# Optimization experiments

Measured on AMD Instinct MI355X. Metric: run time of the kernel, lower is better.

The kernel has to match this reference:

```python
import jax, jax.numpy as jnp
import numpy as np

T = 16000        # signal length
N1 = 120         # first-order filters (J=12, Q=10)
NPSI2 = 14       # second-order filterbank size (Q2=1)
NPAIR = 553      # second-order coefficients -> 120 + 553 = 673 channels
SUB1 = 8         # subsample U1 before order 2
T2 = T // SUB1   # 2000
STR1 = 1000      # lowpass stride at length T  -> 16 output samples
STR2 = T2 // (T // STR1)  # 125 -> 16 output samples
LOG_EPS = 1e-6
BN_EPS = 1e-5


def _gauss_hat(N, xi, sigma):
    om = np.arange(N) / N
    return np.exp(-((om - xi) ** 2) / (2.0 * sigma ** 2)).astype(np.float32)


def _filterbank():
    Q = 10.0
    xi1 = 0.45 * 2.0 ** (-np.arange(N1) / Q)
    sig1 = np.maximum(xi1 * 0.1, 2.0 / T)
    psi1 = np.stack([_gauss_hat(T, x, s) for x, s in zip(xi1, sig1)])
    phi1 = _gauss_hat(T, 0.0, 0.4 / STR1)
    xi2 = 0.45 * 2.0 ** (-np.arange(NPSI2, dtype=np.float64))
    sig2 = np.maximum(xi2 * 0.2, 2.0 / T2)
    psi2 = np.stack([_gauss_hat(T2, x, s) for x, s in zip(xi2, sig2)])
    phi2 = _gauss_hat(T2, 0.0, 0.4 / STR2)
    pairs = [(i, j) for i in range(N1) for j in range(NPSI2) if xi2[j] < xi1[i] / 2.0]
    pairs = pairs[:NPAIR]
    assert len(pairs) == NPAIR
    pi1 = np.array([p[0] for p in pairs], np.int32)
    pi2 = np.array([p[1] for p in pairs], np.int32)
    return psi1, phi1, psi2, phi2, pi1, pi2


def setup_inputs():
    key = jax.random.key(0)
    ks = jax.random.split(key, 8)
    psi1, phi1, psi2, phi2, pi1, pi2 = _filterbank()
    B = 32
    inp = {
        "x": jax.random.normal(ks[0], (B, 1, T), jnp.float32),
        "psi1_hat": jnp.asarray(psi1),
        "phi1_hat": jnp.asarray(phi1),
        "psi2_hat": jnp.asarray(psi2),
        "phi2_hat": jnp.asarray(phi2),
        "gamma": jnp.ones((673,), jnp.float32),
        "beta": jnp.zeros((673,), jnp.float32),
        "W1": jax.random.normal(ks[1], (300, 673), jnp.float32) * 0.04,
        "b1": jnp.zeros((300,), jnp.float32),
        "W2": jax.random.normal(ks[2], (90, 300), jnp.float32) * 0.06,
        "b2": jnp.zeros((90,), jnp.float32),
        "W3": jax.random.normal(ks[3], (35, 90), jnp.float32) * 0.1,
        "b3": jnp.zeros((35,), jnp.float32),
        "pair_i1": jnp.asarray(pi1),
        "pair_i2": jnp.asarray(pi2),
    }
    return inp


def reference(x, psi1_hat, phi1_hat, psi2_hat, phi2_hat, gamma, beta,
              W1, b1, W2, b2, W3, b3, pair_i1, pair_i2):
    xs = x.squeeze(1)                                       # [B, T]
    Xf = jnp.fft.fft(xs)                                    # [B, T] c64
    # --- order 1: wavelet conv (freq-domain), modulus ---
    U1 = jnp.abs(jnp.fft.ifft(Xf[:, None, :] * psi1_hat[None]))        # [B, N1, T]
    # S1 = lowpass(U1) subsampled to 16 samples
    S1 = jnp.real(jnp.fft.ifft(jnp.fft.fft(U1) * phi1_hat))[..., ::STR1]  # [B, N1, 16]
    # --- order 2 on subsampled U1 ---
    U1sf = jnp.fft.fft(U1[..., ::SUB1])                     # [B, N1, T2]
    U2 = jnp.abs(jnp.fft.ifft(U1sf[:, pair_i1, :] * psi2_hat[pair_i2]))  # [B, NPAIR, T2]
    S2 = jnp.real(jnp.fft.ifft(jnp.fft.fft(U2) * phi2_hat))[..., ::STR2]  # [B, NPAIR, 16]
    S = jnp.concatenate([S1, S2], axis=1)                   # [B, 673, 16]
    # log-abs + temporal mean pooling
    f = jnp.mean(jnp.log(jnp.abs(S) + LOG_EPS), axis=-1)    # [B, 673]
    # BatchNorm1d (training mode: batch statistics)
    mu = jnp.mean(f, axis=0)
    var = jnp.var(f, axis=0)
    f = (f - mu) / jnp.sqrt(var + BN_EPS) * gamma + beta
    # MLP head
    h = jax.nn.relu(f @ W1.T + b1)
    h = jax.nn.relu(h @ W2.T + b2)
    return jax.nn.log_softmax(h @ W3.T + b3, axis=-1)
```

## Files before the change

### kernel.cpp

```cpp
#include <hip/hip_runtime.h>
#include <math.h>

typedef float2 cf;

__device__ __forceinline__ cf cadd(cf a, cf b){ return make_float2(a.x+b.x, a.y+b.y); }
__device__ __forceinline__ cf csub(cf a, cf b){ return make_float2(a.x-b.x, a.y-b.y); }
__device__ __forceinline__ cf cmul(cf a, cf b){ return make_float2(a.x*b.x - a.y*b.y, a.x*b.y + a.y*b.x); }

__device__ __forceinline__ int SW(int i){ return i ^ ((i>>4)&15); }
#define AT(x) s[SW(x)]
#define WFENCE asm volatile("" ::: "memory")

template<bool WAVE> __device__ __forceinline__ void SYf(){
  if constexpr (WAVE) { WFENCE; } else __syncthreads();
}

__device__ __forceinline__ int devB(int i){
  int jm = i/10 + 2;
  double kc = 900.0*exp2((double)(-jm));
  double sg = fmax(180.0*exp2((double)(-jm)), 2.0);
  return min(2000, (int)ceil(kc + 6.5*sg) + 1);
}

template<int N, int L, bool INV>
__device__ __forceinline__ void stage_r2(cf* __restrict__ s, const cf* __restrict__ tw, int tid, int nt){
  constexpr int Ls = L/2, nbf = N/2, tws = 16000/L;
  for (int q = tid; q < nbf; q += nt){
    int blk = q / Ls, j = q - blk*Ls;
    int base = blk*L + j;
    cf w1 = tw[tws*j]; if (INV) w1.y = -w1.y;
    if (!INV){
      cf a = AT(base), b = AT(base+Ls);
      AT(base) = cadd(a,b);
      AT(base+Ls) = cmul(csub(a,b), w1);
    } else {
      cf a = AT(base), b = cmul(AT(base+Ls), w1);
      AT(base) = cadd(a,b);
      AT(base+Ls) = csub(a,b);
    }
  }
}

template<int N, int L, bool INV>
__device__ __forceinline__ void stage_r4(cf* __restrict__ s, const cf* __restrict__ tw, int tid, int nt){
  constexpr int Ls = L/4, nbf = N/4, tws = 16000/L;
  for (int q = tid; q < nbf; q += nt){
    int blk = q / Ls, j = q - blk*Ls;
    int base = blk*L + j;
    cf w1 = tw[tws*j]; if (INV) w1.y = -w1.y;
    cf w2 = cmul(w1,w1), w3 = cmul(w2,w1);
    if (!INV){
      cf y0=AT(base), y1=AT(base+Ls), y2=AT(base+2*Ls), y3=AT(base+3*Ls);
      cf t0=cadd(y0,y2), t1=csub(y0,y2), t2=cadd(y1,y3), t3=csub(y1,y3);
      AT(base)      = cadd(t0,t2);
      AT(base+Ls)   = cmul(make_float2(t1.x + t3.y, t1.y - t3.x), w1);
      AT(base+2*Ls) = cmul(csub(t0,t2), w2);
      AT(base+3*Ls) = cmul(make_float2(t1.x - t3.y, t1.y + t3.x), w3);
    } else {
      cf z0=AT(base);
      cf z1=cmul(AT(base+Ls),   w1);
      cf z2=cmul(AT(base+2*Ls), w2);
      cf z3=cmul(AT(base+3*Ls), w3);
      cf t0=cadd(z0,z2), t1=csub(z0,z2), t2=cadd(z1,z3), t3=csub(z1,z3);
      AT(base)      = cadd(t0,t2);
      AT(base+Ls)   = make_float2(t1.x - t3.y, t1.y + t3.x);
      AT(base+2*Ls) = csub(t0,t2);
      AT(base+3*Ls) = make_float2(t1.x + t3.y, t1.y - t3.x);
    }
  }
}

template<int N, int L, bool INV>
__device__ __forceinline__ void stage_r5(cf* __restrict__ s, const cf* __restrict__ tw, int tid, int nt){
  constexpr int Ls = L/5, nbf = N/5, tws = 16000/L;
  const float C1 = 0.30901699437494742f, S1c = 0.95105651629515357f;
  const float C2 = -0.80901699437494745f, S2c = 0.58778525229247314f;
  for (int q = tid; q < nbf; q += nt){
    int blk = q / Ls, j = q - blk*Ls;
    int base = blk*L + j;
    cf w1 = tw[tws*j]; if (INV) w1.y = -w1.y;
    cf w2 = cmul(w1,w1), w3 = cmul(w2,w1), w4 = cmul(w2,w2);
    if (!INV){
      cf y0=AT(base), y1=AT(base+Ls), y2=AT(base+2*Ls), y3=AT(base+3*Ls), y4=AT(base+4*Ls);
      cf t1=cadd(y1,y4), t2=csub(y1,y4), t3=cadd(y2,y3), t4=csub(y2,y3);
      cf z0 = cadd(y0, cadd(t1,t3));
      cf m1 = make_float2(y0.x + C1*t1.x + C2*t3.x, y0.y + C1*t1.y + C2*t3.y);
      cf m2 = make_float2(y0.x + C2*t1.x + C1*t3.x, y0.y + C2*t1.y + C1*t3.y);
      cf wa = make_float2(S1c*t2.x + S2c*t4.x, S1c*t2.y + S2c*t4.y);
      cf wb = make_float2(S2c*t2.x - S1c*t4.x, S2c*t2.y - S1c*t4.y);
      cf o1 = make_float2(m1.x + wa.y, m1.y - wa.x);
      cf o4 = make_float2(m1.x - wa.y, m1.y + wa.x);
      cf o2 = make_float2(m2.x + wb.y, m2.y - wb.x);
      cf o3 = make_float2(m2.x - wb.y, m2.y + wb.x);
      AT(base) = z0;
      AT(base+Ls)   = cmul(o1,w1);
      AT(base+2*Ls) = cmul(o2,w2);
      AT(base+3*Ls) = cmul(o3,w3);
      AT(base+4*Ls) = cmul(o4,w4);
    } else {
      cf z0=AT(base);
      cf z1=cmul(AT(base+Ls),   w1);
      cf z2=cmul(AT(base+2*Ls), w2);
      cf z3=cmul(AT(base+3*Ls), w3);
      cf z4=cmul(AT(base+4*Ls), w4);
      cf t1=cadd(z1,z4), t2=csub(z1,z4), t3=cadd(z2,z3), t4=csub(z2,z3);
      cf y0 = cadd(z0, cadd(t1,t3));
      cf m1 = make_float2(z0.x + C1*t1.x + C2*t3.x, z0.y + C1*t1.y + C2*t3.y);
      cf m2 = make_float2(z0.x + C2*t1.x + C1*t3.x, z0.y + C2*t1.y + C1*t3.y);
      cf wa = make_float2(S1c*t2.x + S2c*t4.x, S1c*t2.y + S2c*t4.y);
      cf wb = make_float2(S2c*t2.x - S1c*t4.x, S2c*t2.y - S1c*t4.y);
      AT(base)      = y0;
      AT(base+Ls)   = make_float2(m1.x - wa.y, m1.y + wa.x);
      AT(base+2*Ls) = make_float2(m2.x - wb.y, m2.y + wb.x);
      AT(base+3*Ls) = make_float2(m2.x + wb.y, m2.y - wb.x);
      AT(base+4*Ls) = make_float2(m1.x + wa.y, m1.y - wa.x);
    }
  }
}

template<int N, int L, bool INV>
__device__ __forceinline__ void stage_r8(cf* __restrict__ s, const cf* __restrict__ tw, int tid, int nt){
  constexpr int Ls = L/8, nbf = N/8, tws = 16000/L;
  const float RC = 0.70710678118654752f;
  for (int q = tid; q < nbf; q += nt){
    int blk = q / Ls, j = q - blk*Ls;
    int base = blk*L + j;
    cf w1 = tw[tws*j]; if (INV) w1.y = -w1.y;
    cf w2 = cmul(w1,w1), w3 = cmul(w2,w1), w4 = cmul(w2,w2);
    cf w5 = cmul(w4,w1), w6 = cmul(w3,w3), w7 = cmul(w4,w3);
    if (!INV){
      cf y0=AT(base), y1=AT(base+Ls), y2=AT(base+2*Ls), y3=AT(base+3*Ls);
      cf y4=AT(base+4*Ls), y5=AT(base+5*Ls), y6=AT(base+6*Ls), y7=AT(base+7*Ls);
      cf b0=cadd(y0,y4), b1=csub(y0,y4);
      cf b2=cadd(y2,y6), b3=csub(y2,y6);
      cf b4=cadd(y1,y5), b5=csub(y1,y5);
      cf b6=cadd(y3,y7), b7=csub(y3,y7);
      cf r3 = make_float2(b3.y, -b3.x);
      cf r7 = make_float2(b7.y, -b7.x);
      cf c0=cadd(b0,b2), c1=csub(b0,b2);
      cf c2=cadd(b1,r3), c3=csub(b1,r3);
      cf c4=cadd(b4,b6), c5=csub(b4,b6);
      cf c6=cadd(b5,r7), c7=csub(b5,r7);
      cf r5 = make_float2(c5.y, -c5.x);
      cf wc6 = make_float2(RC*(c6.x + c6.y), RC*(c6.y - c6.x));
      cf wc7 = make_float2(RC*(c7.y - c7.x), RC*(-c7.y - c7.x));
      AT(base)      = cadd(c0,c4);
      AT(base+Ls)   = cmul(cadd(c2,wc6), w1);
      AT(base+2*Ls) = cmul(cadd(c1,r5),  w2);
      AT(base+3*Ls) = cmul(cadd(c3,wc7), w3);
      AT(base+4*Ls) = cmul(csub(c0,c4),  w4);
      AT(base+5*Ls) = cmul(csub(c2,wc6), w5);
      AT(base+6*Ls) = cmul(csub(c1,r5),  w6);
      AT(base+7*Ls) = cmul(csub(c3,wc7), w7);
    } else {
      cf z0=AT(base);
      cf z1=cmul(AT(base+Ls),   w1);
      cf z2=cmul(AT(base+2*Ls), w2);
      cf z3=cmul(AT(base+3*Ls), w3);
      cf z4=cmul(AT(base+4*Ls), w4);
      cf z5=cmul(AT(base+5*Ls), w5);
      cf z6=cmul(AT(base+6*Ls), w6);
      cf z7=cmul(AT(base+7*Ls), w7);
      cf b0=cadd(z0,z4), b1=csub(z0,z4);
      cf b2=cadd(z2,z6), b3=csub(z2,z6);
      cf b4=cadd(z1,z5), b5=csub(z1,z5);
      cf b6=cadd(z3,z7), b7=csub(z3,z7);
      cf r3 = make_float2(-b3.y, b3.x);
      cf r7 = make_float2(-b7.y, b7.x);
      cf c0=cadd(b0,b2), c1=csub(b0,b2);
      cf c2=cadd(b1,r3), c3=csub(b1,r3);
      cf c4=cadd(b4,b6), c5=csub(b4,b6);
      cf c6=cadd(b5,r7), c7=csub(b5,r7);
      cf r5 = make_float2(-c5.y, c5.x);
      cf wc6 = make_float2(RC*(c6.x - c6.y), RC*(c6.x + c6.y));
      cf wc7 = make_float2(RC*(-c7.x - c7.y), RC*(c7.x - c7.y));
      AT(base)      = cadd(c0,c4);
      AT(base+Ls)   = cadd(c2,wc6);
      AT(base+2*Ls) = cadd(c1,r5);
      AT(base+3*Ls) = cadd(c3,wc7);
      AT(base+4*Ls) = csub(c0,c4);
      AT(base+5*Ls) = csub(c2,wc6);
      AT(base+6*Ls) = csub(c1,r5);
      AT(base+7*Ls) = csub(c3,wc7);
    }
  }
}

template<bool INV>
__device__ void fft16000(cf* s, const cf* tw, int tid, int nt){
  if (!INV){
    stage_r5<16000,16000,false>(s,tw,tid,nt); __syncthreads();
    stage_r5<16000, 3200,false>(s,tw,tid,nt); __syncthreads();
    stage_r5<16000,  640,false>(s,tw,tid,nt); __syncthreads();
    stage_r8<16000,  128,false>(s,tw,tid,nt); __syncthreads();
    stage_r4<16000,   16,false>(s,tw,tid,nt); __syncthreads();
    stage_r4<16000,    4,false>(s,tw,tid,nt); __syncthreads();
  } else {
    stage_r4<16000,    4,true >(s,tw,tid,nt); __syncthreads();
    stage_r4<16000,   16,true >(s,tw,tid,nt); __syncthreads();
    stage_r8<16000,  128,true >(s,tw,tid,nt); __syncthreads();
    stage_r5<16000,  640,true >(s,tw,tid,nt); __syncthreads();
    stage_r5<16000, 3200,true >(s,tw,tid,nt); __syncthreads();
    stage_r5<16000,16000,true >(s,tw,tid,nt); __syncthreads();
  }
}

template<bool INV>
__device__ void fft2000(cf* s, const cf* tw, int tid, int nt){
  if (!INV){
    stage_r5<2000,2000,false>(s,tw,tid,nt); __syncthreads();
    stage_r5<2000, 400,false>(s,tw,tid,nt); __syncthreads();
    stage_r5<2000,  80,false>(s,tw,tid,nt); __syncthreads();
    stage_r4<2000,  16,false>(s,tw,tid,nt); __syncthreads();
    stage_r4<2000,   4,false>(s,tw,tid,nt); __syncthreads();
  } else {
    stage_r4<2000,   4,true >(s,tw,tid,nt); __syncthreads();
    stage_r4<2000,  16,true >(s,tw,tid,nt); __syncthreads();
    stage_r5<2000,  80,true >(s,tw,tid,nt); __syncthreads();
    stage_r5<2000, 400,true >(s,tw,tid,nt); __syncthreads();
    stage_r5<2000,2000,true >(s,tw,tid,nt); __syncthreads();
  }
}

__device__ void fft8000i(cf* s, const cf* tw, int tid, int nt){
  stage_r8<8000,   8,true>(s,tw,tid,nt); __syncthreads();
  stage_r8<8000,  64,true>(s,tw,tid,nt); __syncthreads();
  stage_r5<8000, 320,true>(s,tw,tid,nt); __syncthreads();
  stage_r5<8000,1600,true>(s,tw,tid,nt); __syncthreads();
  stage_r5<8000,8000,true>(s,tw,tid,nt); __syncthreads();
}
__device__ void fft4000i(cf* s, const cf* tw, int tid, int nt){
  stage_r4<4000,   4,true>(s,tw,tid,nt); __syncthreads();
  stage_r8<4000,  32,true>(s,tw,tid,nt); __syncthreads();
  stage_r5<4000, 160,true>(s,tw,tid,nt); __syncthreads();
  stage_r5<4000, 800,true>(s,tw,tid,nt); __syncthreads();
  stage_r5<4000,4000,true>(s,tw,tid,nt); __syncthreads();
}
__device__ void fft500i(cf* s, const cf* tw, int tid, int nt){
  stage_r4<500,  4,true>(s,tw,tid,nt); __syncthreads();
  stage_r5<500, 20,true>(s,tw,tid,nt); __syncthreads();
  stage_r5<500,100,true>(s,tw,tid,nt); __syncthreads();
  stage_r5<500,500,true>(s,tw,tid,nt); __syncthreads();
}
__device__ void fft1000i(cf* s, const cf* tw, int tid, int nt){
  stage_r8<1000,   8,true>(s,tw,tid,nt); __syncthreads();
  stage_r5<1000,  40,true>(s,tw,tid,nt); __syncthreads();
  stage_r5<1000, 200,true>(s,tw,tid,nt); __syncthreads();
  stage_r5<1000,1000,true>(s,tw,tid,nt); __syncthreads();
}
__device__ __forceinline__ void fft250w(cf* s, const cf* tw, int lane){
  stage_r2<250,  2,true>(s,tw,lane,64); WFENCE;
  stage_r5<250, 10,true>(s,tw,lane,64); WFENCE;
  stage_r5<250, 50,true>(s,tw,lane,64); WFENCE;
  stage_r5<250,250,true>(s,tw,lane,64); WFENCE;
}
__device__ __forceinline__ void fft125w(cf* s, const cf* tw, int lane){
  stage_r5<125,  5,true>(s,tw,lane,64); WFENCE;
  stage_r5<125, 25,true>(s,tw,lane,64); WFENCE;
  stage_r5<125,125,true>(s,tw,lane,64); WFENCE;
}

template<int M, bool INV, bool WAVE>
__device__ __forceinline__ void fftg(cf* s, const cf* tw, int tid, int nt){
  if constexpr (M==2000){
    if constexpr (INV){
      stage_r4<2000,4,true>(s,tw,tid,nt); SYf<WAVE>();
      stage_r4<2000,16,true>(s,tw,tid,nt); SYf<WAVE>();
      stage_r5<2000,80,true>(s,tw,tid,nt); SYf<WAVE>();
      stage_r5<2000,400,true>(s,tw,tid,nt); SYf<WAVE>();
      stage_r5<2000,2000,true>(s,tw,tid,nt); SYf<WAVE>();
    } else {
      stage_r5<2000,2000,false>(s,tw,tid,nt); SYf<WAVE>();
      stage_r5<2000,400,false>(s,tw,tid,nt); SYf<WAVE>();
      stage_r5<2000,80,false>(s,tw,tid,nt); SYf<WAVE>();
      stage_r4<2000,16,false>(s,tw,tid,nt); SYf<WAVE>();
      stage_r4<2000,4,false>(s,tw,tid,nt); SYf<WAVE>();
    }
  } else if constexpr (M==1600){
    if constexpr (INV){
      stage_r8<1600,8,true>(s,tw,tid,nt); SYf<WAVE>();
      stage_r8<1600,64,true>(s,tw,tid,nt); SYf<WAVE>();
      stage_r5<1600,320,true>(s,tw,tid,nt); SYf<WAVE>();
      stage_r5<1600,1600,true>(s,tw,tid,nt); SYf<WAVE>();
    } else {
      stage_r5<1600,1600,false>(s,tw,tid,nt); SYf<WAVE>();
      stage_r5<1600,320,false>(s,tw,tid,nt); SYf<WAVE>();
      stage_r8<1600,64,false>(s,tw,tid,nt); SYf<WAVE>();
      stage_r8<1600,8,false>(s,tw,tid,nt); SYf<WAVE>();
    }
  } else if constexpr (M==640){
    if constexpr (INV){
      stage_r4<640,4,true>(s,tw,tid,nt); SYf<WAVE>();
      stage_r4<640,16,true>(s,tw,tid,nt); SYf<WAVE>();
      stage_r8<640,128,true>(s,tw,tid,nt); SYf<WAVE>();
      stage_r5<640,640,true>(s,tw,tid,nt); SYf<WAVE>();
    } else {
      stage_r5<640,640,false>(s,tw,tid,nt); SYf<WAVE>();
      stage_r8<640,128,false>(s,tw,tid,nt); SYf<WAVE>();
      stage_r4<640,16,false>(s,tw,tid,nt); SYf<WAVE>();
      stage_r4<640,4,false>(s,tw,tid,nt); SYf<WAVE>();
    }
  } else if constexpr (M==320){
    if constexpr (INV){
      stage_r8<320,8,true>(s,tw,tid,nt); SYf<WAVE>();
      stage_r8<320,64,true>(s,tw,tid,nt); SYf<WAVE>();
      stage_r5<320,320,true>(s,tw,tid,nt); SYf<WAVE>();
    } else {
      stage_r5<320,320,false>(s,tw,tid,nt); SYf<WAVE>();
      stage_r8<320,64,false>(s,tw,tid,nt); SYf<WAVE>();
      stage_r8<320,8,false>(s,tw,tid,nt); SYf<WAVE>();
    }
  } else if constexpr (M==200){
    if constexpr (INV){
      stage_r8<200,8,true>(s,tw,tid,nt); SYf<WAVE>();
      stage_r5<200,40,true>(s,tw,tid,nt); SYf<WAVE>();
      stage_r5<200,200,true>(s,tw,tid,nt); SYf<WAVE>();
    } else {
      stage_r5<200,200,false>(s,tw,tid,nt); SYf<WAVE>();
      stage_r5<200,40,false>(s,tw,tid,nt); SYf<WAVE>();
      stage_r8<200,8,false>(s,tw,tid,nt); SYf<WAVE>();
    }
  } else {
    if constexpr (INV){
      stage_r4<160,4,true>(s,tw,tid,nt); SYf<WAVE>();
      stage_r8<160,32,true>(s,tw,tid,nt); SYf<WAVE>();
      stage_r5<160,160,true>(s,tw,tid,nt); SYf<WAVE>();
    } else {
      stage_r5<160,160,false>(s,tw,tid,nt); SYf<WAVE>();
      stage_r8<160,32,false>(s,tw,tid,nt); SYf<WAVE>();
      stage_r4<160,4,false>(s,tw,tid,nt); SYf<WAVE>();
    }
  }
}

__device__ __forceinline__ int pos16000(int k){
  int k0=k%5; k/=5; int k1=k%5; k/=5; int k2=k%5; k/=5;
  int k3=k&7; k>>=3; int k4=k&3; k>>=2;
  return k0*3200 + k1*640 + k2*128 + k3*16 + k4*4 + k;
}
__device__ __forceinline__ int pos8000(int k){
  int k0=k%5; k/=5; int k1=k%5; k/=5; int k2=k%5; k/=5;
  int k3=k&7, k4=k>>3;
  return k0*1600 + k1*320 + k2*64 + k3*8 + k4;
}
__device__ __forceinline__ int pos4000(int k){
  int k0=k%5; k/=5; int k1=k%5; k/=5; int k2=k%5; k/=5;
  int k3=k&7, k4=k>>3;
  return k0*800 + k1*160 + k2*32 + k3*4 + k4;
}
__device__ __forceinline__ int pos2000(int k){
  int k0=k%5; k/=5; int k1=k%5; k/=5; int k2=k%5; k/=5;
  int k3=k&3, k4=k>>2;
  return k0*400 + k1*80 + k2*16 + k3*4 + k4;
}
__device__ __forceinline__ int pos1600(int k){
  int k0=k%5; k/=5; int k1=k%5; k/=5;
  int k2=k&7; k>>=3;
  return k0*320 + k1*64 + k2*8 + k;
}
__device__ __forceinline__ int pos1000(int k){
  int k0=k%5; k/=5; int k1=k%5; k/=5; int k2=k%5; k/=5;
  return k0*200 + k1*40 + k2*8 + k;
}
__device__ __forceinline__ int pos640(int k){
  int k0=k%5; k/=5;
  int k1=k&7; k>>=3; int k2=k&3; k>>=2;
  return k0*128 + k1*16 + k2*4 + k;
}
__device__ __forceinline__ int pos500(int k){
  int k0=k%5; k/=5; int k1=k%5; k/=5; int k2=k%5; k/=5;
  return k0*100 + k1*20 + k2*4 + k;
}
__device__ __forceinline__ int pos320(int k){
  int k0=k%5; k/=5;
  int k1=k&7; k>>=3;
  return k0*64 + k1*8 + k;
}
__device__ __forceinline__ int pos250(int k){
  int k0=k%5; k/=5; int k1=k%5; k/=5; int k2=k%5; k/=5;
  return k0*50 + k1*10 + k2*2 + k;
}
__device__ __forceinline__ int pos125(int k){
  int k0=k%5; k/=5; int k1=k%5; k/=5;
  return k0*25 + k1*5 + k;
}
__device__ __forceinline__ int pos200(int k){
  int k0=k%5; k/=5; int k1=k%5; k/=5;
  return k0*40 + k1*8 + k;
}
__device__ __forceinline__ int pos160(int k){
  int k0=k%5; k/=5;
  int k1=k&7; k>>=3;
  return k0*32 + k1*4 + k;
}

template<int M> __device__ __forceinline__ int posM(int k){
  if constexpr (M==16000) return pos16000(k);
  else if constexpr (M==8000) return pos8000(k);
  else if constexpr (M==4000) return pos4000(k);
  else return pos2000(k);
}
template<int M> __device__ __forceinline__ int posN(int k){
  if constexpr (M==2000) return pos2000(k);
  else if constexpr (M==1600) return pos1600(k);
  else if constexpr (M==640) return pos640(k);
  else if constexpr (M==320) return pos320(k);
  else if constexpr (M==200) return pos200(k);
  else return pos160(k);
}
template<int M> __device__ __forceinline__ void fftM_inv(cf* s, const cf* tw, int tid, int nt){
  if constexpr (M==16000) fft16000<true>(s,tw,tid,nt);
  else if constexpr (M==8000) fft8000i(s,tw,tid,nt);
  else if constexpr (M==4000) fft4000i(s,tw,tid,nt);
  else fft2000<true>(s,tw,tid,nt);
}


__global__ void k_tw(cf* __restrict__ tw){
  int j = blockIdx.x*blockDim.x + threadIdx.x;
  if (j < 16000){
    double a = -6.283185307179586476925286766559 * (double)j / 16000.0;
    tw[j] = make_float2((float)cos(a), (float)sin(a));
  }
}

__global__ void k_btab(const float* __restrict__ phi1, const float* __restrict__ phi2,
                       float* __restrict__ h1g, float* __restrict__ h2g){
  int i = blockIdx.x*blockDim.x + threadIdx.x;
  const double TWO_PI = 6.283185307179586476925286766559;
  if (i < 5201){
    int d = i - 2600;
    double a = 0.0;
    for (int k = 0; k < 64; ++k) a += (double)phi1[k]*cos(TWO_PI*(double)(k*d)/16000.0);
    h1g[i] = (float)(a/16000.0 - (double)phi1[0]/32000.0);
  } else if (i == 5201){
    h1g[5201] = phi1[0]*(1.f/32000.f);
  } else if (i < 5202 + 661){
    int j = i - 5202; int d = j - 330;
    double a = 0.0;
    for (int k = 0; k < 64; ++k) a += (double)phi2[k]*cos(TWO_PI*(double)(k*d)/2000.0);
    h2g[j] = (float)(a/2000.0 - (double)phi2[0]/4000.0);
  } else if (i == 5202 + 661){
    h2g[661] = phi2[0]*(1.f/4000.f);
  }
}

__global__ __launch_bounds__(1024) void k_classify(const int* __restrict__ pi2,
                                                   int* __restrict__ list5, int* __restrict__ list4){
  __shared__ int w5[16], w4[16];
  int p = threadIdx.x;
  for (int t = p; t < 493; t += 1024) list5[t] = 0;
  for (int t = p; t < 60;  t += 1024) list4[t] = 0;
  bool valid = p < 553;
  int j2 = valid ? pi2[p] : 99;
  bool f5 = valid && (j2 >= 5);
  bool f4 = valid && (j2 < 5);
  unsigned long long m5 = __ballot(f5);
  unsigned long long m4 = __ballot(f4);
  int lane = p & 63, wid = p >> 6;
  if (lane == 0){ w5[wid] = __popcll(m5); w4[wid] = __popcll(m4); }
  __syncthreads();
  if (valid){
    int b5 = 0, b4 = 0;
    for (int w = 0; w < wid; ++w){ b5 += w5[w]; b4 += w4[w]; }
    unsigned long long lm = (1ull << lane) - 1ull;
    if (f5) list5[b5 + __popcll(m5 & lm)] = p;
    if (f4) list4[b4 + __popcll(m4 & lm)] = p;
  }
}

__global__ __launch_bounds__(1024) void k_fftx(const float* __restrict__ x, cf* __restrict__ Xf,
                                               const cf* __restrict__ tw){
  extern __shared__ cf s[];
  int b = blockIdx.x;
  int tid = threadIdx.x, nt = blockDim.x;
  for (int n = tid; n < 16000; n += nt) AT(n) = make_float2(x[b*16000 + n], 0.f);
  __syncthreads();
  fft16000<false>(s, tw, tid, nt);
  for (int k = tid; k < 16000; k += nt) Xf[b*16000 + k] = AT(pos16000(k));
}

template<int M, int ST, int NF, int I0, int NT>
__global__ __launch_bounds__(NT) void kf(const cf* __restrict__ Xf, const float* __restrict__ psi1,
                                         const float* __restrict__ h1g, const cf* __restrict__ tw,
                                         cf* __restrict__ U1sf, float* __restrict__ S1){
  extern __shared__ cf s[];
  constexpr int NW = NT/64;
  int b = blockIdx.x / NF;
  int i = I0 + (blockIdx.x - b*NF);
  int tid = threadIdx.x, wid = tid>>6, lane = tid&63;
  double x1 = 0.45 * exp2((double)(-i) / 10.0);
  double kc = 16000.0 * x1;
  double sg = fmax(1600.0 * x1, 2.0);
  int k0 = max(0, (int)floor(kc - 6.5*sg));
  int k1 = min(16000, (int)ceil(kc + 6.5*sg) + 1);
  int W = k1 - k0;
  for (int n = tid; n < M; n += NT) s[n] = make_float2(0.f, 0.f);
  __syncthreads();
  const cf* X = Xf + (size_t)b*16000 + k0;
  const float* P = psi1 + (size_t)i*16000 + k0;
  for (int j = tid; j < W; j += NT){
    cf v = X[j]; float pf = P[j];
    int pp = posM<M>(j);
    AT(pp) = make_float2(v.x*pf, v.y*pf);
  }
  __syncthreads();
  fftM_inv<M>(s, tw, tid, NT);
  constexpr int R = (M + NT - 1)/NT;
  float mreg[R]; float tsum = 0.f;
  const float inv = 1.f/16000.f;
  #pragma unroll
  for (int r = 0; r < R; ++r){
    int n = tid + r*NT;
    if (n < M){ cf v = AT(n); mreg[r] = sqrtf(v.x*v.x + v.y*v.y)*inv; tsum += mreg[r]; }
    else mreg[r] = 0.f;
  }
  float* fl = (float*)s;
  float* part = (float*)(s + M);
  __syncthreads();
  #pragma unroll
  for (int r = 0; r < R; ++r){ int n = tid + r*NT; if (n < M) fl[n] = mreg[r]; }
  #pragma unroll
  for (int o = 32; o > 0; o >>= 1) tsum += __shfl_xor(tsum, o);
  if (lane == 0) part[wid] = tsum;
  __syncthreads();
  if (tid == 0){ float tt = 0.f; for (int w = 0; w < NW; ++w) tt += part[w]; part[NW] = tt; }
  __syncthreads();
  float stot = part[NW];
  float c1 = h1g[5201];
  for (int t = wid; t < 16; t += NW){
    int mlo = (1000*t - 2600)/ST;
    int mhi = (1000*t + 2600)/ST;
    float acc = 0.f;
    for (int m = mlo + lane; m <= mhi; m += 64){
      int mm = m; if (mm < 0) mm += M; else if (mm >= M) mm -= M;
      acc = fmaf(fl[mm], h1g[1000*t - m*ST + 2600], acc);
    }
    #pragma unroll
    for (int o = 32; o > 0; o >>= 1) acc += __shfl_xor(acc, o);
    if (lane == 0) S1[((size_t)b*120 + i)*16 + t] = (float)ST*(acc + c1*stot);
  }
  constexpr int K = 8/ST;
  float d0 = fl[tid*K];
  float d1 = 0.f;
  { int m2 = tid + 1024; if (m2 < 2000) d1 = fl[m2*K]; }
  __syncthreads();
  AT(tid) = make_float2(d0, 0.f);
  { int m2 = tid + 1024; if (m2 < 2000) AT(m2) = make_float2(d1, 0.f); }
  __syncthreads();
  fft2000<false>(s, tw, tid, NT);
  int B = devB(i);
  cf* out = U1sf + ((size_t)b*120 + i)*2000;
  for (int k = tid; k < B; k += NT) out[k] = AT(pos2000(k));
}

template<int M, int NF, int I0>
__global__ __launch_bounds__(256) void k_n2(const cf* __restrict__ Xf, const float* __restrict__ psi1,
                                            const float* __restrict__ phi1, const cf* __restrict__ tw,
                                            cf* __restrict__ U1sf, float* __restrict__ S1){
  extern __shared__ cf s[];
  int b = blockIdx.x / NF;
  int i = I0 + (blockIdx.x - b*NF);
  int tid = threadIdx.x, wid = tid>>6, lane = tid&63;
  double x1 = 0.45 * exp2((double)(-i)/10.0);
  double kc = 16000.0*x1, sg = fmax(1600.0*x1, 2.0);
  int k0 = max(0,(int)floor(kc-6.5*sg));
  int k1 = min(16000,(int)ceil(kc+6.5*sg)+1);
  int W = k1-k0;
  for (int n = tid; n < M; n += 256) s[n] = make_float2(0.f,0.f);
  __syncthreads();
  const cf* X = Xf + (size_t)b*16000 + k0;
  const float* P = psi1 + (size_t)i*16000 + k0;
  for (int j = tid; j < W; j += 256){
    cf v = X[j]; float pf = P[j];
    AT(posN<M>(j)) = make_float2(v.x*pf, v.y*pf);
  }
  __syncthreads();
  fftg<M,true,false>(s,tw,tid,256);
  for (int n = tid; n < M; n += 256){
    cf v = AT(n);
    AT(n) = make_float2(sqrtf(v.x*v.x+v.y*v.y)*(1.f/16000.f), 0.f);
  }
  __syncthreads();
  fftg<M,false,false>(s,tw,tid,256);
  {
    int k = lane;
    cf g = AT(posN<M>(k));
    float ph = phi1[k];
    float gx = g.x*ph, gy = g.y*ph;
    float* S1o = S1 + ((size_t)b*120+i)*16;
    for (int r = 0; r < 4; ++r){
      int t = wid + 4*r;
      cf e = tw[1000*((k*t)&15)];
      float val = gx*e.x + gy*e.y;
      #pragma unroll
      for (int o = 32; o > 0; o >>= 1) val += __shfl_xor(val, o);
      if (lane == 0) S1o[t] = val*(1.f/(float)M);
    }
  }
  int B = devB(i);
  const float sc = 2000.f/(float)M;
  cf* out = U1sf + ((size_t)b*120+i)*2000;
  for (int k = tid; k < B; k += 256){
    cf v = AT(posN<M>(k));
    out[k] = make_float2(v.x*sc, v.y*sc);
  }
}

template<int M, int SPAD, int NF, int I0, int WPB>
__global__ __launch_bounds__(WPB*64) void k_nw2(const cf* __restrict__ Xf, const float* __restrict__ psi1,
                                                const float* __restrict__ phi1, const cf* __restrict__ tw,
                                                cf* __restrict__ U1sf, float* __restrict__ S1){
  extern __shared__ cf sh[];
  int wid = threadIdx.x >> 6, lane = threadIdx.x & 63;
  int q = blockIdx.x*WPB + wid;
  int filt = q >> 5, b = q & 31;
  int i = I0 + filt;
  cf* s = sh + wid*SPAD;
  double x1 = 0.45 * exp2((double)(-i)/10.0);
  double kc = 16000.0*x1, sg = fmax(1600.0*x1, 2.0);
  int k0 = max(0,(int)floor(kc-6.5*sg));
  int k1 = min(16000,(int)ceil(kc+6.5*sg)+1);
  int W = k1-k0;
  for (int n = lane; n < SPAD; n += 64) s[n] = make_float2(0.f,0.f);
  WFENCE;
  const cf* X = Xf + (size_t)b*16000 + k0;
  const float* P = psi1 + (size_t)i*16000 + k0;
  for (int j = lane; j < W; j += 64){
    cf v = X[j]; float pf = P[j];
    AT(posN<M>(j)) = make_float2(v.x*pf, v.y*pf);
  }
  WFENCE;
  fftg<M,true,true>(s,tw,lane,64);
  for (int n = lane; n < M; n += 64){
    cf v = AT(n);
    AT(n) = make_float2(sqrtf(v.x*v.x+v.y*v.y)*(1.f/16000.f), 0.f);
  }
  WFENCE;
  fftg<M,false,true>(s,tw,lane,64);
  {
    int k = lane;
    cf g = AT(posN<M>(k));
    float ph = phi1[k];
    float gx = g.x*ph, gy = g.y*ph;
    float* S1o = S1 + ((size_t)b*120+i)*16;
    for (int t = 0; t < 16; ++t){
      cf e = tw[1000*((k*t)&15)];
      float val = gx*e.x + gy*e.y;
      #pragma unroll
      for (int o = 32; o > 0; o >>= 1) val += __shfl_xor(val, o);
      if (lane == 0) S1o[t] = val*(1.f/(float)M);
    }
  }
  int B = devB(i);
  const float sc = 2000.f/(float)M;
  cf* out = U1sf + ((size_t)b*120+i)*2000;
  for (int k = lane; k < B; k += 64){
    cf v = AT(posN<M>(k));
    out[k] = make_float2(v.x*sc, v.y*sc);
  }
}

__global__ __launch_bounds__(256) void k_sec5(const cf* __restrict__ U1sf, const float* __restrict__ psi2,
                                              const float* __restrict__ h2g, const cf* __restrict__ tw,
                                              const int* __restrict__ pi1, const int* __restrict__ pi2,
                                              const int* __restrict__ list5, float* __restrict__ S2){
  __shared__ cf sall[4*256];
  __shared__ float flall[4*256];
  int wid = threadIdx.x >> 6, lane = threadIdx.x & 63;
  int q = blockIdx.x*4 + wid;
  int p = list5[q >> 5];
  int b = q & 31;
  int i1 = pi1[p], j2 = pi2[p];
  cf* s = sall + wid*256;
  float* fl2 = flall + wid*256;
  int M2  = (j2 >= 6) ? 125 : 250;
  int s2l = (j2 >= 6) ? 4 : 3;
  double xc = exp2((double)(-j2));
  double kc = 900.0*xc, sg = fmax(180.0*xc, 2.0);
  int k0 = max(0, (int)floor(kc - 6.5*sg));
  int k1 = min(2000, (int)ceil(kc + 6.5*sg) + 1);
  int W = k1 - k0;
  for (int n = lane; n < 256; n += 64) s[n] = make_float2(0.f, 0.f);
  WFENCE;
  const cf* U = U1sf + (size_t)(b*120 + i1)*2000 + k0;
  const float* F = psi2 + j2*2000 + k0;
  for (int j = lane; j < W; j += 64){
    cf v = U[j]; float f = F[j];
    int pp = (M2 == 125) ? pos125(j) : pos250(j);
    AT(pp) = make_float2(v.x*f, v.y*f);
  }
  WFENCE;
  if (M2 == 125) fft125w(s, tw, lane); else fft250w(s, tw, lane);
  float tsum = 0.f;
  #pragma unroll
  for (int r = 0; r < 4; ++r){
    int n = lane + r*64;
    if (n < M2){
      cf v = AT(n);
      float mg = sqrtf(v.x*v.x + v.y*v.y)*(1.f/2000.f);
      fl2[n] = mg; tsum += mg;
    }
  }
  WFENCE;
  #pragma unroll
  for (int o = 32; o > 0; o >>= 1) tsum += __shfl_xor(tsum, o);
  float stot = tsum;
  float c2 = h2g[661];
  float scale = (float)(1 << s2l);
  float* S2o = S2 + (size_t)(b*553 + p)*16;
  int g16 = lane >> 4, li = lane & 15;
  for (int r = 0; r < 4; ++r){
    int t = g16*4 + r;
    int x0 = 125*t - 330, x1b = 125*t + 330;
    int mlo = (x0 + ((1<<s2l)-1)) >> s2l;
    int mhi = x1b >> s2l;
    float acc = 0.f;
    for (int m = mlo + li; m <= mhi; m += 16){
      int mm = m; if (mm < 0) mm += M2; else if (mm >= M2) mm -= M2;
      acc = fmaf(fl2[mm], h2g[125*t - (m << s2l) + 330], acc);
    }
    #pragma unroll
    for (int o = 8; o > 0; o >>= 1) acc += __shfl_xor(acc, o);
    if (li == 0) S2o[t] = scale*(acc + c2*stot);
  }
}

__global__ __launch_bounds__(128) void k_secbig(const cf* __restrict__ U1sf, const float* __restrict__ psi2,
                                                const float* __restrict__ h2g, const cf* __restrict__ tw,
                                                const int* __restrict__ pi1, const int* __restrict__ pi2,
                                                const int* __restrict__ list4, float* __restrict__ S2){
  extern __shared__ cf s[];
  float* fl2 = (float*)(s + 2000);
  float* part = fl2 + 2000;
  int p = list4[blockIdx.x >> 5];
  int b = blockIdx.x & 31;
  int tid = threadIdx.x, wid = tid>>6, lane = tid&63;
  int i1 = pi1[p], j2 = pi2[p];
  int M2, s2l;
  if (j2 == 4){ M2 = 500;  s2l = 2; }
  else if (j2 == 3){ M2 = 1000; s2l = 1; }
  else { M2 = 2000; s2l = 0; }
  int ST2 = 1 << s2l;
  double xc = exp2((double)(-j2));
  double kc = 900.0*xc, sg = fmax(180.0*xc, 2.0);
  int k0 = max(0, (int)floor(kc - 6.5*sg));
  int k1 = min(2000, (int)ceil(kc + 6.5*sg) + 1);
  int W = k1 - k0;
  int M2r = (M2 + 15) & ~15;
  for (int n = tid; n < M2r; n += 128) s[n] = make_float2(0.f, 0.f);
  __syncthreads();
  const cf* U = U1sf + (size_t)(b*120 + i1)*2000 + k0;
  const float* F = psi2 + j2*2000 + k0;
  for (int j = tid; j < W; j += 128){
    cf v = U[j]; float f = F[j];
    int pp;
    if (M2 == 500) pp = pos500(j);
    else if (M2 == 1000) pp = pos1000(j);
    else pp = pos2000(j);
    AT(pp) = make_float2(v.x*f, v.y*f);
  }
  __syncthreads();
  if (M2 == 500) fft500i(s, tw, tid, 128);
  else if (M2 == 1000) fft1000i(s, tw, tid, 128);
  else fft2000<true>(s, tw, tid, 128);
  float tsum = 0.f;
  for (int n = tid; n < M2; n += 128){
    cf v = AT(n);
    float mg = sqrtf(v.x*v.x + v.y*v.y)*(1.f/2000.f);
    fl2[n] = mg; tsum += mg;
  }
  #pragma unroll
  for (int o = 32; o > 0; o >>= 1) tsum += __shfl_xor(tsum, o);
  if (lane == 0) part[wid] = tsum;
  __syncthreads();
  float stot = part[0] + part[1];
  float c2 = h2g[661];
  float* S2o = S2 + (size_t)(b*553 + p)*16;
  for (int r = 0; r < 8; ++r){
    int t = wid + (r<<1);
    int mlo = (125*t - 330 + ST2 - 1) >> s2l;
    int mhi = (125*t + 330) >> s2l;
    float acc = 0.f;
    for (int m = mlo + lane; m <= mhi; m += 64){
      int mm = m; if (mm < 0) mm += M2; else if (mm >= M2) mm -= M2;
      acc = fmaf(fl2[mm], h2g[125*t - m*ST2 + 330], acc);
    }
    #pragma unroll
    for (int o = 32; o > 0; o >>= 1) acc += __shfl_xor(acc, o);
    if (lane == 0) S2o[t] = (float)ST2*(acc + c2*stot);
  }
}

__global__ __launch_bounds__(64) void k_fbn(const float* __restrict__ S1, const float* __restrict__ S2,
                                            const float* __restrict__ g, const float* __restrict__ be,
                                            float* __restrict__ fn){
  int j = blockIdx.x;
  int b = threadIdx.x;
  float f = 0.f;
  if (b < 32){
    const float* src = (j < 120) ? (S1 + (b*120 + j)*16) : (S2 + (b*553 + (j-120))*16);
    float acc = 0.f;
    #pragma unroll
    for (int t = 0; t < 16; ++t) acc += logf(fabsf(src[t]) + 1e-6f);
    f = acc * (1.f/16.f);
  }
  float mu = f;
  #pragma unroll
  for (int o = 16; o > 0; o >>= 1) mu += __shfl_xor(mu, o);
  mu *= (1.f/32.f);
  float d = f - mu;
  float v = d*d;
  #pragma unroll
  for (int o = 16; o > 0; o >>= 1) v += __shfl_xor(v, o);
  v *= (1.f/32.f);
  float is = g[j] / sqrtf(v + 1e-5f);
  if (b < 32) fn[b*673 + j] = d*is + be[j];
}

__global__ __launch_bounds__(512) void k_mlp1(const float* __restrict__ fn,
                                              const float* __restrict__ W1, const float* __restrict__ b1,
                                              float* __restrict__ h1o){
  int task = blockIdx.x*8 + (threadIdx.x >> 6);
  int lane = threadIdx.x & 63;
  if (task >= 32*300) return;
  int b = task / 300, r = task - b*300;
  const float* f = fn + b*673;
  const float* w = W1 + r*673;
  float acc = 0.f;
  for (int k = lane; k < 673; k += 64) acc = fmaf(f[k], w[k], acc);
  #pragma unroll
  for (int o = 32; o > 0; o >>= 1) acc += __shfl_down(acc, o);
  if (lane == 0) h1o[b*300 + r] = fmaxf(acc + b1[r], 0.f);
}

__global__ __launch_bounds__(512) void k_mlp2(const float* __restrict__ h1,
                                              const float* __restrict__ W2, const float* __restrict__ b2,
                                              float* __restrict__ h2o){
  int task = blockIdx.x*8 + (threadIdx.x >> 6);
  int lane = threadIdx.x & 63;
  if (task >= 32*90) return;
  int b = task / 90, r = task - b*90;
  const float* h = h1 + b*300;
  const float* w = W2 + r*300;
  float acc = 0.f;
  for (int k = lane; k < 300; k += 64) acc = fmaf(h[k], w[k], acc);
  #pragma unroll
  for (int o = 32; o > 0; o >>= 1) acc += __shfl_down(acc, o);
  if (lane == 0) h2o[b*90 + r] = fmaxf(acc + b2[r], 0.f);
}

__global__ __launch_bounds__(256) void k_mlp3(const float* __restrict__ h2,
                                              const float* __restrict__ W3, const float* __restrict__ b3,
                                              float* __restrict__ out){
  __shared__ float lg[35];
  int b = blockIdx.x;
  int tid = threadIdx.x, wid = tid >> 6, lane = tid & 63;
  for (int r = wid; r < 35; r += 4){
    float acc = 0.f;
    for (int k = lane; k < 90; k += 64) acc = fmaf(h2[b*90 + k], W3[r*90 + k], acc);
    #pragma unroll
    for (int o = 32; o > 0; o >>= 1) acc += __shfl_down(acc, o);
    if (lane == 0) lg[r] = acc + b3[r];
  }
  __syncthreads();
  if (tid < 64){
    float v = (tid < 35) ? lg[tid] : -1e30f;
    float mx = v;
    #pragma unroll
    for (int o = 32; o > 0; o >>= 1) mx = fmaxf(mx, __shfl_xor(mx, o));
    float e = (tid < 35) ? expf(v - mx) : 0.f;
    float se = e;
    #pragma unroll
    for (int o = 32; o > 0; o >>= 1) se += __shfl_xor(se, o);
    if (tid < 35) out[b*35 + tid] = v - mx - logf(se);
  }
}


extern "C" void kernel_launch(void* const* d_in, const int* in_sizes, int n_in,
                              void* d_out, int out_size, void* d_ws, size_t ws_size,
                              hipStream_t stream){
  const float* x     = (const float*)d_in[0];
  const float* psi1  = (const float*)d_in[1];
  const float* phi1  = (const float*)d_in[2];
  const float* psi2  = (const float*)d_in[3];
  const float* phi2  = (const float*)d_in[4];
  const float* gamma = (const float*)d_in[5];
  const float* beta  = (const float*)d_in[6];
  const float* W1    = (const float*)d_in[7];
  const float* b1    = (const float*)d_in[8];
  const float* W2    = (const float*)d_in[9];
  const float* b2    = (const float*)d_in[10];
  const float* W3    = (const float*)d_in[11];
  const float* b3    = (const float*)d_in[12];
  const int*   pi1   = (const int*)d_in[13];
  const int*   pi2   = (const int*)d_in[14];

  char* ws = (char*)d_ws;
  constexpr size_t o_tw = 0;
  constexpr size_t o_Xf = o_tw + (size_t)16000*sizeof(cf);
  constexpr size_t o_U  = o_Xf + (size_t)32*16000*sizeof(cf);
  constexpr size_t o_S1 = o_U  + (size_t)3840*2000*sizeof(cf);
  constexpr size_t o_S2 = o_S1 + (size_t)3840*16*sizeof(float);
  constexpr size_t o_l5 = o_S2 + (size_t)17696*16*sizeof(float);
  constexpr size_t o_l4 = o_l5 + (size_t)512*sizeof(int);
  constexpr size_t o_fn = o_l4 + (size_t)64*sizeof(int);
  constexpr size_t o_h1 = o_fn + (size_t)32*673*sizeof(float);
  constexpr size_t o_h2 = o_h1 + (size_t)5202*sizeof(float);
  constexpr size_t o_m1 = o_h2 + (size_t)662*sizeof(float);
  constexpr size_t o_m2 = o_m1 + (size_t)32*300*sizeof(float);

  cf*    tw    = (cf*)(ws + o_tw);
  cf*    Xf    = (cf*)(ws + o_Xf);
  cf*    U1sf  = (cf*)(ws + o_U);
  float* S1b   = (float*)(ws + o_S1);
  float* S2b   = (float*)(ws + o_S2);
  int*   list5 = (int*)(ws + o_l5);
  int*   list4 = (int*)(ws + o_l4);
  float* fnbuf = (float*)(ws + o_fn);
  float* h1g   = (float*)(ws + o_h1);
  float* h2g   = (float*)(ws + o_h2);
  float* m1buf = (float*)(ws + o_m1);
  float* m2buf = (float*)(ws + o_m2);

  hipFuncSetAttribute((const void*)k_fftx, hipFuncAttributeMaxDynamicSharedMemorySize, 131072);
  hipFuncSetAttribute((const void*)kf<16000,1,13, 0,1024>, hipFuncAttributeMaxDynamicSharedMemorySize, 131072);
  hipFuncSetAttribute((const void*)kf< 8000,2,10,13,1024>, hipFuncAttributeMaxDynamicSharedMemorySize, 131072);

  k_tw<<<63, 256, 0, stream>>>(tw);
  k_btab<<<23, 256, 0, stream>>>(phi1, phi2, h1g, h2g);
  k_classify<<<1, 1024, 0, stream>>>(pi2, list5, list4);
  k_fftx<<<32, 1024, 128000, stream>>>(x, Xf, tw);
  kf<16000,1,13, 0,1024><<<32*13, 1024, 16000*8 + 17*4, stream>>>(Xf, psi1, h1g, tw, U1sf, S1b);
  kf< 8000,2,10,13,1024><<<32*10, 1024,  8000*8 + 17*4, stream>>>(Xf, psi1, h1g, tw, U1sf, S1b);
  kf< 4000,4,10,23,1024><<<32*10, 1024,  4000*8 + 17*4, stream>>>(Xf, psi1, h1g, tw, U1sf, S1b);
  k_n2<2000,10,33><<<32*10, 256, 2000*8, stream>>>(Xf, psi1, phi1, tw, U1sf, S1b);
  k_n2<1600,10,43><<<32*10, 256, 1600*8, stream>>>(Xf, psi1, phi1, tw, U1sf, S1b);
  k_nw2<640,640,10,53,4><<< 80, 256, 4*640*8, stream>>>(Xf, psi1, phi1, tw, U1sf, S1b);
  k_nw2<320,320,10,63,8><<< 40, 512, 8*320*8, stream>>>(Xf, psi1, phi1, tw, U1sf, S1b);
  k_nw2<200,208,10,73,8><<< 40, 512, 8*208*8, stream>>>(Xf, psi1, phi1, tw, U1sf, S1b);
  k_nw2<160,160,37,83,8><<<148, 512, 8*160*8, stream>>>(Xf, psi1, phi1, tw, U1sf, S1b);
  k_sec5<<<(493*32)/4, 256, 0, stream>>>(U1sf, psi2, h2g, tw, pi1, pi2, list5, S2b);
  k_secbig<<<60*32, 128, 2000*8 + 2000*4 + 4*4, stream>>>(U1sf, psi2, h2g, tw, pi1, pi2, list4, S2b);
  k_fbn<<<673, 64, 0, stream>>>(S1b, S2b, gamma, beta, fnbuf);
  k_mlp1<<<1200, 512, 0, stream>>>(fnbuf, W1, b1, m1buf);
  k_mlp2<<<360, 512, 0, stream>>>(m1buf, W2, b2, m2buf);
  k_mlp3<<<32, 256, 0, stream>>>(m2buf, W3, b3, (float*)d_out);
}
```

Baseline: 343.1 us.

## Split input FFT into four radix-4 decimated 4000-point FFTs per batch

```diff
diff --git a/kernel.cpp b/kernel.cpp
--- a/kernel.cpp
+++ b/kernel.cpp
@@ -236,6 +236,13 @@
   stage_r5<4000, 800,true>(s,tw,tid,nt); __syncthreads();
   stage_r5<4000,4000,true>(s,tw,tid,nt); __syncthreads();
 }
+__device__ void fft4000f(cf* s, const cf* tw, int tid, int nt){
+  stage_r5<4000,4000,false>(s,tw,tid,nt); __syncthreads();
+  stage_r5<4000, 800,false>(s,tw,tid,nt); __syncthreads();
+  stage_r5<4000, 160,false>(s,tw,tid,nt); __syncthreads();
+  stage_r8<4000,  32,false>(s,tw,tid,nt); __syncthreads();
+  stage_r4<4000,   4,false>(s,tw,tid,nt); __syncthreads();
+}
 __device__ void fft500i(cf* s, const cf* tw, int tid, int nt){
   stage_r4<500,  4,true>(s,tw,tid,nt); __syncthreads();
   stage_r5<500, 20,true>(s,tw,tid,nt); __syncthreads();
@@ -469,15 +476,27 @@
   }
 }
 
-__global__ __launch_bounds__(1024) void k_fftx(const float* __restrict__ x, cf* __restrict__ Xf,
+__global__ __launch_bounds__(512) void k_fftx4(const float* __restrict__ x, cf* __restrict__ Xf,
                                                const cf* __restrict__ tw){
   extern __shared__ cf s[];
-  int b = blockIdx.x;
-  int tid = threadIdx.x, nt = blockDim.x;
-  for (int n = tid; n < 16000; n += nt) AT(n) = make_float2(x[b*16000 + n], 0.f);
-  __syncthreads();
-  fft16000<false>(s, tw, tid, nt);
-  for (int k = tid; k < 16000; k += nt) Xf[b*16000 + k] = AT(pos16000(k));
+  int blk = blockIdx.x;
+  int b = blk >> 2, r = blk & 3;
+  int tid = threadIdx.x;
+  const float* xb = x + (size_t)b*16000;
+  for (int j = tid; j < 4000; j += 512){
+    float x0 = xb[j], x1 = xb[j+4000], x2 = xb[j+8000], x3 = xb[j+12000];
+    cf f;
+    if (r == 0)      f = make_float2(x0 + x1 + x2 + x3, 0.f);
+    else if (r == 1) f = make_float2(x0 - x2, x3 - x1);
+    else if (r == 2) f = make_float2(x0 - x1 + x2 - x3, 0.f);
+    else             f = make_float2(x0 - x2, x1 - x3);
+    cf y = (r == 0) ? f : cmul(f, tw[j*r]);
+    AT(j) = y;
+  }
+  __syncthreads();
+  fft4000f(s, tw, tid, 512);
+  cf* out = Xf + (size_t)b*16000 + r;
+  for (int m = tid; m < 4000; m += 512) out[4*m] = AT(pos4000(m));
 }
 
 template<int M, int ST, int NF, int I0, int NT>
@@ -924,14 +943,13 @@
   float* m1buf = (float*)(ws + o_m1);
   float* m2buf = (float*)(ws + o_m2);
 
-  hipFuncSetAttribute((const void*)k_fftx, hipFuncAttributeMaxDynamicSharedMemorySize, 131072);
   hipFuncSetAttribute((const void*)kf<16000,1,13, 0,1024>, hipFuncAttributeMaxDynamicSharedMemorySize, 131072);
   hipFuncSetAttribute((const void*)kf< 8000,2,10,13,1024>, hipFuncAttributeMaxDynamicSharedMemorySize, 131072);
 
   k_tw<<<63, 256, 0, stream>>>(tw);
   k_btab<<<23, 256, 0, stream>>>(phi1, phi2, h1g, h2g);
   k_classify<<<1, 1024, 0, stream>>>(pi2, list5, list4);
-  k_fftx<<<32, 1024, 128000, stream>>>(x, Xf, tw);
+  k_fftx4<<<128, 512, 4000*8, stream>>>(x, Xf, tw);
   kf<16000,1,13, 0,1024><<<32*13, 1024, 16000*8 + 17*4, stream>>>(Xf, psi1, h1g, tw, U1sf, S1b);
   kf< 8000,2,10,13,1024><<<32*10, 1024,  8000*8 + 17*4, stream>>>(Xf, psi1, h1g, tw, U1sf, S1b);
   kf< 4000,4,10,23,1024><<<32*10, 1024,  4000*8 + 17*4, stream>>>(Xf, psi1, h1g, tw, U1sf, S1b);
```

After: 335.5 us. -2.2%, faster.
